# Kernel optimization log

Measured on AMD Instinct MI355X. Metric: run time of the kernel, lower is better.

Reference implementation:

```python
import jax, jax.numpy as jnp
import numpy as np

N_QUBITS = 6
N_LAYERS = 2
SHORT_W = 64
LONG_W = 256
BATCH = 16384


def setup_inputs() -> dict:
    key = jax.random.key(0)
    ks = jax.random.split(key, 15)
    d = {}
    d['xs'] = jax.random.normal(ks[0], (BATCH, 1, SHORT_W), jnp.float32)
    d['xl'] = jax.random.normal(ks[1], (BATCH, 1, LONG_W), jnp.float32)
    d['conv_s_w'] = jax.random.normal(ks[2], (16, 1, 3), jnp.float32) * 0.3
    d['conv_s_b'] = jax.random.normal(ks[3], (16,), jnp.float32) * 0.1
    d['lin_s_w'] = jax.random.normal(ks[4], (N_QUBITS, 16 * SHORT_W), jnp.float32) * 0.03
    d['lin_s_b'] = jax.random.normal(ks[5], (N_QUBITS,), jnp.float32) * 0.1
    d['conv_l_w'] = jax.random.normal(ks[6], (16, 1, 5), jnp.float32) * 0.3
    d['conv_l_b'] = jax.random.normal(ks[7], (16,), jnp.float32) * 0.1
    d['lin_l_w'] = jax.random.normal(ks[8], (N_QUBITS, 16 * LONG_W // 2), jnp.float32) * 0.02
    d['lin_l_b'] = jax.random.normal(ks[9], (N_QUBITS,), jnp.float32) * 0.1
    d['q_weights'] = jax.random.normal(ks[10], (N_LAYERS, N_QUBITS, 3), jnp.float32)
    d['fc1_w'] = jax.random.normal(ks[11], (8, N_QUBITS), jnp.float32) * 0.3
    d['fc1_b'] = jax.random.normal(ks[12], (8,), jnp.float32) * 0.1
    d['fc2_w'] = jax.random.normal(ks[13], (1, 8), jnp.float32) * 0.3
    d['fc2_b'] = jax.random.normal(ks[14], (1,), jnp.float32) * 0.1
    return d


def _conv1d(x, w, b, pad):
    # x: [B,C,W], w: [O,I,K]
    y = jax.lax.conv_general_dilated(x, w, (1,), [(pad, pad)],
                                     dimension_numbers=('NCH', 'OIH', 'NCH'))
    return y + b[None, :, None]


def _apply_1q(state, gate, wire):
    # state: [B,2,2,2,2,2,2]; gate: [2,2] (shared) or [B,2,2] (per-sample)
    s = jnp.moveaxis(state, wire + 1, -1)
    if gate.ndim == 2:
        s = jnp.einsum('...a,ca->...c', s, gate)
    else:
        s = jnp.einsum('b...a,bca->b...c', s, gate)
    return jnp.moveaxis(s, -1, wire + 1)


def _cnot(state, c, t):
    ax_c, ax_t = c + 1, t + 1
    s0 = jnp.take(state, 0, axis=ax_c)
    s1 = jnp.take(state, 1, axis=ax_c)
    t_ax = ax_t - 1 if ax_t > ax_c else ax_t
    s1 = jnp.flip(s1, axis=t_ax)  # X on target when control=1
    return jnp.stack([s0, s1], axis=ax_c)


def _rot(phi, theta, omega):
    # PennyLane Rot = RZ(omega) @ RY(theta) @ RZ(phi)
    c, s = jnp.cos(theta / 2), jnp.sin(theta / 2)
    ep = jnp.exp(-0.5j * (phi + omega).astype(jnp.complex64))
    em = jnp.exp(-0.5j * (phi - omega).astype(jnp.complex64))
    return jnp.array([[0j, 0j], [0j, 0j]]) + jnp.stack([
        jnp.stack([ep * c, -jnp.conj(em) * s]),
        jnp.stack([em * s, jnp.conj(ep) * c])])


def _quantum(f, qw):
    # f: [B, n_qubits] angles-features; qw: [L, n, 3]
    B, n = f.shape
    state = jnp.zeros((B,) + (2,) * n, jnp.complex64)
    state = state.at[(slice(None),) + (0,) * n].set(1.0)
    # RY(pi * f_j) encoding, per-sample gates
    theta = (jnp.pi * f) / 2
    c, s = jnp.cos(theta), jnp.sin(theta)  # [B,n]
    for j in range(n):
        g = jnp.stack([jnp.stack([c[:, j], -s[:, j]], -1),
                       jnp.stack([s[:, j], c[:, j]], -1)], -2).astype(jnp.complex64)
        state = _apply_1q(state, g, j)
    # StronglyEntanglingLayers: Rot on each wire, then CNOT ring with range r
    L = qw.shape[0]
    for l in range(L):
        for j in range(n):
            g = _rot(qw[l, j, 0], qw[l, j, 1], qw[l, j, 2]).astype(jnp.complex64)
            state = _apply_1q(state, g, j)
        r = l % (n - 1) + 1
        for j in range(n):
            state = _cnot(state, j, (j + r) % n)
    # <Z_k> expectations from probabilities
    p = jnp.real(state * jnp.conj(state))  # [B,2,...,2]
    outs = []
    for k in range(n):
        axes = tuple(a for a in range(1, n + 1) if a != k + 1)
        marg = jnp.sum(p, axis=axes)  # [B,2]
        outs.append(marg[:, 0] - marg[:, 1])
    return jnp.stack(outs, axis=-1).astype(jnp.float32)


def reference(xs, xl, conv_s_w, conv_s_b, lin_s_w, lin_s_b,
              conv_l_w, conv_l_b, lin_l_w, lin_l_b,
              q_weights, fc1_w, fc1_b, fc2_w, fc2_b):
    B = xs.shape[0]
    # short branch: Conv1d(1,16,3,pad=1) -> ReLU -> Flatten -> Linear
    hs = jax.nn.relu(_conv1d(xs, conv_s_w, conv_s_b, 1))  # [B,16,SHORT_W]
    fs = hs.reshape(B, -1) @ lin_s_w.T + lin_s_b          # [B,6]
    # long branch: Conv1d(1,16,5,pad=2) -> ReLU -> MaxPool(2) -> Flatten -> Linear
    hl = jax.nn.relu(_conv1d(xl, conv_l_w, conv_l_b, 2))  # [B,16,LONG_W]
    hl = hl.reshape(B, 16, hl.shape[-1] // 2, 2).max(-1)  # MaxPool1d(2)
    fl = hl.reshape(B, -1) @ lin_l_w.T + lin_l_b          # [B,6]
    f = (fs + fl) / 2
    # quantum layer runs on detached values in the original (no grad flow)
    q = _quantum(jax.lax.stop_gradient(f), jax.lax.stop_gradient(q_weights))
    h = jax.nn.relu(q @ fc1_w.T + fc1_b)
    return h @ fc2_w.T + fc2_b  # [B,1]
```

## Files before the change

### kernel.cpp

```cpp
#include <hip/hip_runtime.h>
#include <math.h>

#define SPW 2
#define WPB 8
#define NTHR (WPB * 64)

__global__ __launch_bounds__(NTHR) void hybridqrc_kernel(
    const float* __restrict__ xs,  const float* __restrict__ xl,
    const float* __restrict__ csw, const float* __restrict__ csb,
    const float* __restrict__ lsw, const float* __restrict__ lsb,
    const float* __restrict__ clw, const float* __restrict__ clb,
    const float* __restrict__ llw, const float* __restrict__ llb,
    const float* __restrict__ qw,  const float* __restrict__ fc1w,
    const float* __restrict__ fc1b,const float* __restrict__ fc2w,
    const float* __restrict__ fc2b,float* __restrict__ out, int B)
{
    __shared__ float llw_s[12288];
    __shared__ float4 gme[24];
    const int tid = threadIdx.x;
#pragma unroll
    for (int idx = 0; idx < 3072; idx += NTHR) {
        int k = idx + tid;
        if (k < 3072)
            reinterpret_cast<float4*>(llw_s)[k] =
                reinterpret_cast<const float4*>(llw)[k];
    }
    if (tid < 24) {
        int g = tid >> 1, bit = tid & 1;
        float phi = qw[g * 3 + 0], th = qw[g * 3 + 1], om = qw[g * 3 + 2];
        float a = 0.5f * (phi + om), b = 0.5f * (phi - om);
        float ca = cosf(a), sa = sinf(a);
        float cb = cosf(b), sb = sinf(b);
        float ct = cosf(0.5f * th), st = sinf(0.5f * th);
        float4 v;
        if (bit) { v.x = ca * ct; v.y =  sa * ct; v.z =  cb * st; v.w = -sb * st; }
        else     { v.x = ca * ct; v.y = -sa * ct; v.z = -cb * st; v.w = -sb * st; }
        gme[tid] = v;
    }
    __syncthreads();

    const int lane = tid & 63;
    const int wave = blockIdx.x * WPB + (tid >> 6);
    const int base = wave * SPW;
    if (base >= B) return;

    int perm0, perm1;
    {
        int y = lane;
#pragma unroll
        for (int j = 5; j >= 0; j--) {
            const int t = (j + 1) % 6;
            y ^= (y & (1 << (5 - j))) ? (1 << (5 - t)) : 0;
        }
        perm0 = y;
        y = lane;
#pragma unroll
        for (int j = 5; j >= 0; j--) {
            const int t = (j + 2) % 6;
            y ^= (y & (1 << (5 - j))) ? (1 << (5 - t)) : 0;
        }
        perm1 = y;
    }

    float acc[SPW][6];
#pragma unroll
    for (int i = 0; i < SPW; i++)
#pragma unroll
        for (int q = 0; q < 6; q++) acc[i][q] = 0.f;

    float xsv[SPW], xm1[SPW], xp1[SPW];
#pragma unroll
    for (int i = 0; i < SPW; i++) xsv[i] = xs[(base + i) * 64 + lane];
#pragma unroll
    for (int i = 0; i < SPW; i++) {
        float lft = __shfl(xsv[i], (lane + 63) & 63, 64);
        float rgt = __shfl(xsv[i], (lane + 1) & 63, 64);
        xm1[i] = (lane == 0)  ? 0.f : lft;
        xp1[i] = (lane == 63) ? 0.f : rgt;
    }
#pragma unroll
    for (int c = 0; c < 16; c++) {
        float w0 = csw[c * 3 + 0], w1 = csw[c * 3 + 1], w2 = csw[c * 3 + 2];
        float bb = csb[c];
        float h[SPW];
#pragma unroll
        for (int i = 0; i < SPW; i++)
            h[i] = fmaxf(0.f, fmaf(w0, xm1[i], fmaf(w1, xsv[i], fmaf(w2, xp1[i], bb))));
#pragma unroll
        for (int q = 0; q < 6; q++) {
            float wv = lsw[q * 1024 + c * 64 + lane];
#pragma unroll
            for (int i = 0; i < SPW; i++) acc[i][q] = fmaf(h[i], wv, acc[i][q]);
        }
    }

    float4 xlv[SPW];
    float l2v[SPW], l1v[SPW], r1v[SPW], r2v[SPW];
#pragma unroll
    for (int i = 0; i < SPW; i++)
        xlv[i] = reinterpret_cast<const float4*>(xl + (size_t)(base + i) * 256)[lane];
#pragma unroll
    for (int i = 0; i < SPW; i++) {
        float a = __shfl(xlv[i].z, (lane + 63) & 63, 64);
        float b = __shfl(xlv[i].w, (lane + 63) & 63, 64);
        float c = __shfl(xlv[i].x, (lane + 1) & 63, 64);
        float d = __shfl(xlv[i].y, (lane + 1) & 63, 64);
        l2v[i] = (lane == 0)  ? 0.f : a;
        l1v[i] = (lane == 0)  ? 0.f : b;
        r1v[i] = (lane == 63) ? 0.f : c;
        r2v[i] = (lane == 63) ? 0.f : d;
    }
#pragma unroll
    for (int c = 0; c < 16; c++) {
        float w0 = clw[c * 5 + 0], w1 = clw[c * 5 + 1], w2 = clw[c * 5 + 2];
        float w3 = clw[c * 5 + 3], w4 = clw[c * 5 + 4];
        float bb = clb[c];
        float p0[SPW], p1[SPW];
#pragma unroll
        for (int i = 0; i < SPW; i++) {
            float vx = xlv[i].x, vy = xlv[i].y, vz = xlv[i].z, vw = xlv[i].w;
            float h0 = fmaf(w0, l2v[i], fmaf(w1, l1v[i], fmaf(w2, vx, fmaf(w3, vy, fmaf(w4, vz, bb)))));
            float h1 = fmaf(w0, l1v[i], fmaf(w1, vx, fmaf(w2, vy, fmaf(w3, vz, fmaf(w4, vw, bb)))));
            float h2 = fmaf(w0, vx, fmaf(w1, vy, fmaf(w2, vz, fmaf(w3, vw, fmaf(w4, r1v[i], bb)))));
            float h3 = fmaf(w0, vy, fmaf(w1, vz, fmaf(w2, vw, fmaf(w3, r1v[i], fmaf(w4, r2v[i], bb)))));
            h0 = fmaxf(h0, 0.f); h1 = fmaxf(h1, 0.f);
            h2 = fmaxf(h2, 0.f); h3 = fmaxf(h3, 0.f);
            p0[i] = fmaxf(h0, h1);
            p1[i] = fmaxf(h2, h3);
        }
#pragma unroll
        for (int q = 0; q < 6; q++) {
            float2 wv = reinterpret_cast<const float2*>(llw_s + q * 2048 + c * 128)[lane];
#pragma unroll
            for (int i = 0; i < SPW; i++)
                acc[i][q] = fmaf(p0[i], wv.x, fmaf(p1[i], wv.y, acc[i][q]));
        }
    }

    float fv[12];
    {
        float v[16];
#pragma unroll
        for (int q = 0; q < 6; q++) { v[q] = acc[0][q]; v[6 + q] = acc[1][q]; }
        v[12] = 0.f; v[13] = 0.f; v[14] = 0.f; v[15] = 0.f;
        {
            const bool hi = lane & 1;
#pragma unroll
            for (int j = 0; j < 8; j++) {
                float snd = hi ? v[j] : v[j + 8];
                float rcv = __shfl_xor(snd, 1, 64);
                float kept = hi ? v[j + 8] : v[j];
                v[j] = kept + rcv;
            }
        }
        {
            const bool hi = lane & 2;
#pragma unroll
            for (int j = 0; j < 4; j++) {
                float snd = hi ? v[j] : v[j + 4];
                float rcv = __shfl_xor(snd, 2, 64);
                float kept = hi ? v[j + 4] : v[j];
                v[j] = kept + rcv;
            }
        }
        {
            const bool hi = lane & 4;
#pragma unroll
            for (int j = 0; j < 2; j++) {
                float snd = hi ? v[j] : v[j + 2];
                float rcv = __shfl_xor(snd, 4, 64);
                float kept = hi ? v[j + 2] : v[j];
                v[j] = kept + rcv;
            }
        }
        {
            const bool hi = lane & 8;
            float snd = hi ? v[0] : v[1];
            float rcv = __shfl_xor(snd, 8, 64);
            float kept = hi ? v[1] : v[0];
            v[0] = kept + rcv;
        }
        float r = v[0];
        r += __shfl_xor(r, 16, 64);
        r += __shfl_xor(r, 32, 64);
        const int rl[12] = {0, 8, 4, 12, 2, 10, 6, 14, 1, 9, 5, 13};
#pragma unroll
        for (int j = 0; j < 12; j++)
            fv[j] = __int_as_float(
                __builtin_amdgcn_readlane(__float_as_int(r), rl[j]));
    }
    float f[SPW][6];
#pragma unroll
    for (int i = 0; i < SPW; i++)
#pragma unroll
        for (int q = 0; q < 6; q++)
            f[i][q] = 0.5f * (fv[i * 6 + q] + lsb[q] + llb[q]);

    float ar[SPW], ai[SPW];
#pragma unroll
    for (int i = 0; i < SPW; i++) { ar[i] = 1.f; ai[i] = 0.f; }
#pragma unroll
    for (int j = 0; j < 6; j++) {
        const int mask = 1 << (5 - j);
#pragma unroll
        for (int i = 0; i < SPW; i++) {
            float th = 1.57079632679489662f * f[i][j];
            float ss = __sinf(th), cc = __cosf(th);
            ar[i] *= (lane & mask) ? ss : cc;
        }
    }

#define APPLY_GATE(L, J) do {                                              \
        const int _mask = 1 << (5 - (J));                                  \
        const int _bit = (lane & _mask) ? 1 : 0;                           \
        float4 g = gme[((L) * 6 + (J)) * 2 + _bit];                        \
        _Pragma("unroll")                                                  \
        for (int i = 0; i < SPW; i++) {                                    \
            float br = __shfl_xor(ar[i], _mask, 64);                       \
            float bi = __shfl_xor(ai[i], _mask, 64);                       \
            float nr = g.x * ar[i] - g.y * ai[i] + g.z * br - g.w * bi;    \
            float ni = g.x * ai[i] + g.y * ar[i] + g.z * bi + g.w * br;    \
            ar[i] = nr; ai[i] = ni;                                        \
        } } while (0)

    APPLY_GATE(0, 0); APPLY_GATE(0, 1); APPLY_GATE(0, 2);
    APPLY_GATE(0, 3); APPLY_GATE(0, 4); APPLY_GATE(0, 5);
#pragma unroll
    for (int i = 0; i < SPW; i++) {
        float pr = __shfl(ar[i], perm0, 64);
        float pi2 = __shfl(ai[i], perm0, 64);
        ar[i] = pr; ai[i] = pi2;
    }
    APPLY_GATE(1, 0); APPLY_GATE(1, 1); APPLY_GATE(1, 2);
    APPLY_GATE(1, 3); APPLY_GATE(1, 4); APPLY_GATE(1, 5);
#pragma unroll
    for (int i = 0; i < SPW; i++) {
        float pr = __shfl(ar[i], perm1, 64);
        float pi2 = __shfl(ai[i], perm1, 64);
        ar[i] = pr; ai[i] = pi2;
    }

    float outv[SPW];
#pragma unroll
    for (int i = 0; i < SPW; i++) {
        float v = ar[i] * ar[i] + ai[i] * ai[i];
#pragma unroll
        for (int m = 1; m < 64; m <<= 1) {
            float pp = __shfl_xor(v, m, 64);
            v = (lane & m) ? (pp - v) : (v + pp);
        }
        float z[6];
#pragma unroll
        for (int k = 0; k < 6; k++)
            z[k] = __int_as_float(
                __builtin_amdgcn_readlane(__float_as_int(v), 32 >> k));
        float o = fc2b[0];
#pragma unroll
        for (int m = 0; m < 8; m++) {
            float h = fc1b[m];
#pragma unroll
            for (int k = 0; k < 6; k++) h = fmaf(fc1w[m * 6 + k], z[k], h);
            h = fmaxf(h, 0.f);
            o = fmaf(fc2w[m], h, o);
        }
        outv[i] = o;
    }

    if (lane == 0) {
#pragma unroll
        for (int i = 0; i < SPW; i++)
            if (base + i < B) out[base + i] = outv[i];
    }
}

extern "C" void kernel_launch(void* const* d_in, const int* in_sizes, int n_in,
                              void* d_out, int out_size, void* d_ws, size_t ws_size,
                              hipStream_t stream) {
    const float* xs   = (const float*)d_in[0];
    const float* xl   = (const float*)d_in[1];
    const float* csw  = (const float*)d_in[2];
    const float* csb  = (const float*)d_in[3];
    const float* lsw  = (const float*)d_in[4];
    const float* lsb  = (const float*)d_in[5];
    const float* clw  = (const float*)d_in[6];
    const float* clb  = (const float*)d_in[7];
    const float* llw  = (const float*)d_in[8];
    const float* llb  = (const float*)d_in[9];
    const float* qw   = (const float*)d_in[10];
    const float* fc1w = (const float*)d_in[11];
    const float* fc1b = (const float*)d_in[12];
    const float* fc2w = (const float*)d_in[13];
    const float* fc2b = (const float*)d_in[14];
    float* out = (float*)d_out;

    const int B = in_sizes[0] / 64;
    const int spb = WPB * SPW;
    const int blocks = (B + spb - 1) / spb;
    hybridqrc_kernel<<<blocks, NTHR, 0, stream>>>(
        xs, xl, csw, csb, lsw, lsb, clw, clb, llw, llb,
        qw, fc1w, fc1b, fc2w, fc2b, out, B);
}
```

Baseline: 116.9 us.

## Stage both linear weights in LDS with float4-interleaved layout and prefetch inputs

Copies both the short-branch and long-branch linear weights into shared memory, rearranged so that each lane reads one float4 covering several channels, which cuts the number of LDS and global load instructions. Input loads for xs and xl are issued before the weight staging and the barrier, so their latency overlaps with that work. Block size doubles to 16 waves and launch bounds add an occupancy hint. In exchange, shared memory per block grows to about 72KB, which may limit blocks per CU, and every block re-stages the full weight set.

```diff
diff --git a/kernel.cpp b/kernel.cpp
--- a/kernel.cpp
+++ b/kernel.cpp
@@ -2,10 +2,10 @@
 #include <math.h>
 
 #define SPW 2
-#define WPB 8
+#define WPB 16
 #define NTHR (WPB * 64)
 
-__global__ __launch_bounds__(NTHR) void hybridqrc_kernel(
+__global__ __launch_bounds__(NTHR, 8) void hybridqrc_kernel(
     const float* __restrict__ xs,  const float* __restrict__ xl,
     const float* __restrict__ csw, const float* __restrict__ csb,
     const float* __restrict__ lsw, const float* __restrict__ lsb,
@@ -15,15 +15,33 @@
     const float* __restrict__ fc1b,const float* __restrict__ fc2w,
     const float* __restrict__ fc2b,float* __restrict__ out, int B)
 {
+    __shared__ float lsw_s[6144];
     __shared__ float llw_s[12288];
     __shared__ float4 gme[24];
     const int tid = threadIdx.x;
-#pragma unroll
-    for (int idx = 0; idx < 3072; idx += NTHR) {
-        int k = idx + tid;
-        if (k < 3072)
-            reinterpret_cast<float4*>(llw_s)[k] =
-                reinterpret_cast<const float4*>(llw)[k];
+    const int lane = tid & 63;
+    const int wave = blockIdx.x * WPB + (tid >> 6);
+    const int base = wave * SPW;
+
+    float xsv[SPW];
+    float4 xlv[SPW];
+#pragma unroll
+    for (int i = 0; i < SPW; i++) {
+        xsv[i] = xs[(base + i) * 64 + lane];
+        xlv[i] = reinterpret_cast<const float4*>(xl + (size_t)(base + i) * 256)[lane];
+    }
+
+#pragma unroll
+    for (int it = 0; it < 6; it++) {
+        int k = it * NTHR + tid;
+        int w = k & 63, c = (k >> 6) & 15, q = k >> 10;
+        lsw_s[(q * 4 + (c >> 2)) * 256 + w * 4 + (c & 3)] = lsw[k];
+    }
+#pragma unroll
+    for (int it = 0; it < 12; it++) {
+        int k = it * NTHR + tid;
+        int j = k & 127, c = (k >> 7) & 15, q = k >> 11;
+        llw_s[(q * 8 + (c >> 1)) * 256 + (j >> 1) * 4 + (c & 1) * 2 + (j & 1)] = llw[k];
     }
     if (tid < 24) {
         int g = tid >> 1, bit = tid & 1;
@@ -39,9 +57,6 @@
     }
     __syncthreads();
 
-    const int lane = tid & 63;
-    const int wave = blockIdx.x * WPB + (tid >> 6);
-    const int base = wave * SPW;
     if (base >= B) return;
 
     int perm0, perm1;
@@ -68,72 +83,82 @@
 #pragma unroll
         for (int q = 0; q < 6; q++) acc[i][q] = 0.f;
 
-    float xsv[SPW], xm1[SPW], xp1[SPW];
-#pragma unroll
-    for (int i = 0; i < SPW; i++) xsv[i] = xs[(base + i) * 64 + lane];
-#pragma unroll
-    for (int i = 0; i < SPW; i++) {
-        float lft = __shfl(xsv[i], (lane + 63) & 63, 64);
-        float rgt = __shfl(xsv[i], (lane + 1) & 63, 64);
-        xm1[i] = (lane == 0)  ? 0.f : lft;
-        xp1[i] = (lane == 63) ? 0.f : rgt;
-    }
-#pragma unroll
-    for (int c = 0; c < 16; c++) {
-        float w0 = csw[c * 3 + 0], w1 = csw[c * 3 + 1], w2 = csw[c * 3 + 2];
-        float bb = csb[c];
-        float h[SPW];
-#pragma unroll
-        for (int i = 0; i < SPW; i++)
-            h[i] = fmaxf(0.f, fmaf(w0, xm1[i], fmaf(w1, xsv[i], fmaf(w2, xp1[i], bb))));
-#pragma unroll
-        for (int q = 0; q < 6; q++) {
-            float wv = lsw[q * 1024 + c * 64 + lane];
-#pragma unroll
-            for (int i = 0; i < SPW; i++) acc[i][q] = fmaf(h[i], wv, acc[i][q]);
-        }
-    }
-
-    float4 xlv[SPW];
-    float l2v[SPW], l1v[SPW], r1v[SPW], r2v[SPW];
-#pragma unroll
-    for (int i = 0; i < SPW; i++)
-        xlv[i] = reinterpret_cast<const float4*>(xl + (size_t)(base + i) * 256)[lane];
-#pragma unroll
-    for (int i = 0; i < SPW; i++) {
-        float a = __shfl(xlv[i].z, (lane + 63) & 63, 64);
-        float b = __shfl(xlv[i].w, (lane + 63) & 63, 64);
-        float c = __shfl(xlv[i].x, (lane + 1) & 63, 64);
-        float d = __shfl(xlv[i].y, (lane + 1) & 63, 64);
-        l2v[i] = (lane == 0)  ? 0.f : a;
-        l1v[i] = (lane == 0)  ? 0.f : b;
-        r1v[i] = (lane == 63) ? 0.f : c;
-        r2v[i] = (lane == 63) ? 0.f : d;
-    }
-#pragma unroll
-    for (int c = 0; c < 16; c++) {
-        float w0 = clw[c * 5 + 0], w1 = clw[c * 5 + 1], w2 = clw[c * 5 + 2];
-        float w3 = clw[c * 5 + 3], w4 = clw[c * 5 + 4];
-        float bb = clb[c];
-        float p0[SPW], p1[SPW];
+    {
+        float xm1[SPW], xp1[SPW];
 #pragma unroll
         for (int i = 0; i < SPW; i++) {
-            float vx = xlv[i].x, vy = xlv[i].y, vz = xlv[i].z, vw = xlv[i].w;
-            float h0 = fmaf(w0, l2v[i], fmaf(w1, l1v[i], fmaf(w2, vx, fmaf(w3, vy, fmaf(w4, vz, bb)))));
-            float h1 = fmaf(w0, l1v[i], fmaf(w1, vx, fmaf(w2, vy, fmaf(w3, vz, fmaf(w4, vw, bb)))));
-            float h2 = fmaf(w0, vx, fmaf(w1, vy, fmaf(w2, vz, fmaf(w3, vw, fmaf(w4, r1v[i], bb)))));
-            float h3 = fmaf(w0, vy, fmaf(w1, vz, fmaf(w2, vw, fmaf(w3, r1v[i], fmaf(w4, r2v[i], bb)))));
-            h0 = fmaxf(h0, 0.f); h1 = fmaxf(h1, 0.f);
-            h2 = fmaxf(h2, 0.f); h3 = fmaxf(h3, 0.f);
-            p0[i] = fmaxf(h0, h1);
-            p1[i] = fmaxf(h2, h3);
-        }
-#pragma unroll
-        for (int q = 0; q < 6; q++) {
-            float2 wv = reinterpret_cast<const float2*>(llw_s + q * 2048 + c * 128)[lane];
-#pragma unroll
-            for (int i = 0; i < SPW; i++)
-                acc[i][q] = fmaf(p0[i], wv.x, fmaf(p1[i], wv.y, acc[i][q]));
+            float lft = __shfl(xsv[i], (lane + 63) & 63, 64);
+            float rgt = __shfl(xsv[i], (lane + 1) & 63, 64);
+            xm1[i] = (lane == 0)  ? 0.f : lft;
+            xp1[i] = (lane == 63) ? 0.f : rgt;
+        }
+        const float4* lsw_s4 = reinterpret_cast<const float4*>(lsw_s);
+#pragma unroll
+        for (int c4 = 0; c4 < 4; c4++) {
+            float h[4][SPW];
+#pragma unroll
+            for (int cc = 0; cc < 4; cc++) {
+                const int c = c4 * 4 + cc;
+                float w0 = csw[c * 3 + 0], w1 = csw[c * 3 + 1], w2 = csw[c * 3 + 2];
+                float bb = csb[c];
+#pragma unroll
+                for (int i = 0; i < SPW; i++)
+                    h[cc][i] = fmaxf(0.f,
+                        fmaf(w0, xm1[i], fmaf(w1, xsv[i], fmaf(w2, xp1[i], bb))));
+            }
+#pragma unroll
+            for (int q = 0; q < 6; q++) {
+                float4 wv = lsw_s4[(q * 4 + c4) * 64 + lane];
+#pragma unroll
+                for (int i = 0; i < SPW; i++)
+                    acc[i][q] = fmaf(h[0][i], wv.x, fmaf(h[1][i], wv.y,
+                                fmaf(h[2][i], wv.z, fmaf(h[3][i], wv.w, acc[i][q]))));
+            }
+        }
+    }
+
+    {
+        float l2v[SPW], l1v[SPW], r1v[SPW], r2v[SPW];
+#pragma unroll
+        for (int i = 0; i < SPW; i++) {
+            float a = __shfl(xlv[i].z, (lane + 63) & 63, 64);
+            float b = __shfl(xlv[i].w, (lane + 63) & 63, 64);
+            float c = __shfl(xlv[i].x, (lane + 1) & 63, 64);
+            float d = __shfl(xlv[i].y, (lane + 1) & 63, 64);
+            l2v[i] = (lane == 0)  ? 0.f : a;
+            l1v[i] = (lane == 0)  ? 0.f : b;
+            r1v[i] = (lane == 63) ? 0.f : c;
+            r2v[i] = (lane == 63) ? 0.f : d;
+        }
+        const float4* llw_s4 = reinterpret_cast<const float4*>(llw_s);
+#pragma unroll
+        for (int c2 = 0; c2 < 8; c2++) {
+            float p0[2][SPW], p1[2][SPW];
+#pragma unroll
+            for (int cc = 0; cc < 2; cc++) {
+                const int c = c2 * 2 + cc;
+                float w0 = clw[c * 5 + 0], w1 = clw[c * 5 + 1], w2 = clw[c * 5 + 2];
+                float w3 = clw[c * 5 + 3], w4 = clw[c * 5 + 4];
+                float bb = clb[c];
+#pragma unroll
+                for (int i = 0; i < SPW; i++) {
+                    float vx = xlv[i].x, vy = xlv[i].y, vz = xlv[i].z, vw = xlv[i].w;
+                    float h0 = fmaf(w0, l2v[i], fmaf(w1, l1v[i], fmaf(w2, vx, fmaf(w3, vy, fmaf(w4, vz, bb)))));
+                    float h1 = fmaf(w0, l1v[i], fmaf(w1, vx, fmaf(w2, vy, fmaf(w3, vz, fmaf(w4, vw, bb)))));
+                    float h2 = fmaf(w0, vx, fmaf(w1, vy, fmaf(w2, vz, fmaf(w3, vw, fmaf(w4, r1v[i], bb)))));
+                    float h3 = fmaf(w0, vy, fmaf(w1, vz, fmaf(w2, vw, fmaf(w3, r1v[i], fmaf(w4, r2v[i], bb)))));
+                    p0[cc][i] = fmaxf(fmaxf(h0, h1), 0.f);
+                    p1[cc][i] = fmaxf(fmaxf(h2, h3), 0.f);
+                }
+            }
+#pragma unroll
+            for (int q = 0; q < 6; q++) {
+                float4 wv = llw_s4[(q * 8 + c2) * 64 + lane];
+#pragma unroll
+                for (int i = 0; i < SPW; i++)
+                    acc[i][q] = fmaf(p0[0][i], wv.x, fmaf(p1[0][i], wv.y,
+                                fmaf(p0[1][i], wv.z, fmaf(p1[1][i], wv.w, acc[i][q]))));
+            }
         }
     }
 
```

After: 119.2 us. No clear change (+2.0%).
